# Optimization experiments

Hardware: AMD Instinct MI355X
Metric: run time of the kernel (lower is better)

Reference implementation:

```python
import jax, jax.numpy as jnp
import numpy as np

D, DEPTH, HEADS, P, IMG = 768, 12, 12, 16, 224
GRID = IMG // P
NTOK = GRID * GRID + 1  # 197
PLEN, NTASK, NCLS = 5, 5, 100
DEEP = (2, 3, 4)
HD = D // HEADS
LN_EPS = 1e-6


def _ln(x, w, b):
    m = x.mean(-1, keepdims=True)
    v = ((x - m) ** 2).mean(-1, keepdims=True)
    return (x - m) * jax.lax.rsqrt(v + LN_EPS) * w + b


def _l2n(x):
    return x * jax.lax.rsqrt(jnp.maximum((x * x).sum(-1, keepdims=True), 1e-12))


def _mlp(x, w1, b1, w2, b2):
    return jax.nn.gelu(x @ w1.T + b1, approximate=False) @ w2.T + b2


def _mha(x, wqkv, bqkv, wp, bp):
    B, N, _ = x.shape
    qkv = (x @ wqkv.T + bqkv).reshape(B, N, 3, HEADS, HD)
    q, k, v = qkv[:, :, 0], qkv[:, :, 1], qkv[:, :, 2]
    a = jax.nn.softmax(jnp.einsum('bnhd,bmhd->bhnm', q * HD ** -0.5, k), -1)
    o = jnp.einsum('bhnm,bmhd->bnhd', a, v).reshape(B, N, D)
    return o @ wp.T + bp


def _block(x, i, p):
    x = x + _mha(_ln(x, p['ln1_w'][i], p['ln1_b'][i]), p['qkv_w'][i], p['qkv_b'][i], p['proj_w'][i], p['proj_b'][i])
    return x + _mlp(_ln(x, p['ln2_w'][i], p['ln2_b'][i]), p['fc1_w'][i], p['fc1_b'][i], p['fc2_w'][i], p['fc2_b'][i])


def _blocks(x, p):
    for i in range(DEPTH):
        x = _block(x, i, p)
    return x


def _deep_block(x, i, li, prompts, p):
    # single-head prefix-prompt attention exactly as written in the torch module,
    # including the (buggy but faithful) transpose(1,2).reshape(B,N,C) scramble
    B, N, _ = x.shape
    nx = _ln(x, p['ln1_w'][i], p['ln1_b'][i])
    qkv = (nx @ p['qkv_w'][i].T + p['qkv_b'][i]).reshape(B, N, 3, D)
    q, k, v = qkv[:, :, 0], qkv[:, :, 1], qkv[:, :, 2]
    k = jnp.concatenate([prompts[:, 2 * li], k], axis=1)
    v = jnp.concatenate([prompts[:, 2 * li + 1], v], axis=1)
    a = jax.nn.softmax(jnp.einsum('bnd,bmd->bnm', q, k) * HD ** -0.5, -1)
    av = jnp.einsum('bnm,bmd->bnd', a, v)
    av = av.swapaxes(1, 2).reshape(B, N, D)
    x = x + (av @ p['proj_w'][i].T + p['proj_b'][i])
    return x + _mlp(_ln(x, p['ln2_w'][i], p['ln2_b'][i]), p['fc1_w'][i], p['fc1_b'][i], p['fc2_w'][i], p['fc2_b'][i])


def _embed(inputs, patch_w, patch_b, cls_token, pos_embed):
    B = inputs.shape[0]
    x = inputs.reshape(B, 3, GRID, P, GRID, P).transpose(0, 2, 4, 1, 3, 5).reshape(B, GRID * GRID, 3 * P * P)
    x = x @ patch_w.T + patch_b
    x = jnp.concatenate([jnp.broadcast_to(cls_token, (B, 1, D)), x], axis=1)
    return x + pos_embed


def _branch_forward(x, sel_main, main_idx, sub_idx, p, main_prompts, sub_prompt, pos_embed, fc_w, fc_b, norm_w, norm_b):
    B = x.shape[0]
    # ---- main branch: per-sample gathered deep prompts ----
    mx = x[main_idx]
    mp = main_prompts[sel_main].reshape(mx.shape[0], 2 * len(DEEP), PLEN, D)
    for i in range(DEPTH):
        if i in DEEP:
            mx = _deep_block(mx, i, DEEP.index(i), mp, p)
        else:
            mx = _block(mx, i, p)
    mx = _ln(mx, norm_w, norm_b)
    mlog = mx[:, 0] @ fc_w.T + fc_b  # fc_norm is Identity in timm vit_base
    # ---- sub branch: prepend sub prompts after cls ----
    sx = x[sub_idx]
    sp = jnp.broadcast_to(sub_prompt[0] + pos_embed[0, 0], (sx.shape[0], PLEN, D))
    sx = jnp.concatenate([sx[:, :1], sp, sx[:, 1:]], axis=1)
    sx = _ln(_blocks(sx, p), norm_w, norm_b)
    slog = sx[:, 1:1 + PLEN].mean(axis=1) @ fc_w.T + fc_b
    # scatter back to per-sample logits (fixed output shape)
    return jnp.zeros((B, NCLS), x.dtype).at[main_idx].set(mlog).at[sub_idx].set(slog)


def setup_inputs() -> dict:
    key = jax.random.key(0)
    ks = iter(jax.random.split(key, 32))
    nk = lambda: next(ks)
    r = lambda shape, sc=0.02: jax.random.normal(nk(), shape, jnp.float32) * sc
    return {
        'inputs': jax.random.normal(nk(), (16, 3, IMG, IMG), jnp.float32),
        'task_id': 4,
        'patch_w': r((D, 3 * P * P)),
        'patch_b': jnp.zeros((D,)),
        'cls_token': r((1, 1, D)),
        'pos_embed': r((1, NTOK, D)),
        'qkv_w': r((DEPTH, 3 * D, D)),
        'qkv_b': jnp.zeros((DEPTH, 3 * D)),
        'proj_w': r((DEPTH, D, D)),
        'proj_b': jnp.zeros((DEPTH, D)),
        'ln1_w': jnp.ones((DEPTH, D)), 'ln1_b': jnp.zeros((DEPTH, D)),
        'ln2_w': jnp.ones((DEPTH, D)), 'ln2_b': jnp.zeros((DEPTH, D)),
        'fc1_w': r((DEPTH, 4 * D, D)),
        'fc1_b': jnp.zeros((DEPTH, 4 * D)),
        'fc2_w': r((DEPTH, D, 4 * D)),
        'fc2_b': jnp.zeros((DEPTH, D)),
        'norm_w': jnp.ones((D,)), 'norm_b': jnp.zeros((D,)),
        'fc_w': r((NCLS, D)),
        'fc_b': jnp.zeros((NCLS,)),
        'main_key': r((NTASK, D), 1.0),
        'sub_key': r((1, D), 1.0),
        'main_prompts': r((NTASK, 1, 2, len(DEEP), PLEN, D), 1.0),
        'sub_prompt': r((1, PLEN, D), 1.0),
    }


def reference(inputs, task_id, patch_w, patch_b, cls_token, pos_embed, qkv_w, qkv_b, proj_w, proj_b,
              ln1_w, ln1_b, ln2_w, ln2_b, fc1_w, fc1_b, fc2_w, fc2_b, norm_w, norm_b, fc_w, fc_b,
              main_key, sub_key, main_prompts, sub_prompt):
    p = dict(qkv_w=qkv_w, qkv_b=qkv_b, proj_w=proj_w, proj_b=proj_b, ln1_w=ln1_w, ln1_b=ln1_b,
             ln2_w=ln2_w, ln2_b=ln2_b, fc1_w=fc1_w, fc1_b=fc1_b, fc2_w=fc2_w, fc2_b=fc2_b)
    x = _embed(inputs, patch_w, patch_b, cls_token, pos_embed)
    # frozen query pass (torch.no_grad in the original)
    query = _ln(_blocks(x, p), norm_w, norm_b)[:, 0]
    # test-time routing: cosine similarity to [main_key[:task_id+1], sub_key]
    cand = jnp.concatenate([main_key[:task_id + 1], sub_key], axis=0)
    sim = _l2n(query) @ _l2n(cand).T
    sel = jnp.argmax(sim, axis=1)  # selection_size == 1
    main_mask = sel <= task_id
    main_idx = jnp.nonzero(main_mask)[0]
    sub_idx = jnp.nonzero(jnp.logical_not(main_mask))[0]
    sel_main = sel[main_idx]
    return _branch_forward(x, sel_main, main_idx, sub_idx, p, main_prompts, sub_prompt, pos_embed,
                           fc_w, fc_b, norm_w, norm_b)
```

## Files before the change

### kernel.cpp

```cpp
#include <hip/hip_runtime.h>
#include <math.h>

#define B_    16
#define NT_   197
#define NS_   202
#define HEADS_ 12
#define DEPTH_ 12
#define NCLS_ 100
#define MROW_ (B_ * NT_)
#define SROW_ (B_ * NS_)
#define CROW_ (MROW_ + SROW_)
#define PAD_  128

typedef __attribute__((ext_vector_type(8))) short short8v;
typedef __attribute__((ext_vector_type(4))) float f32x4;

__device__ __forceinline__ short f2bf(float f){
    unsigned u = __builtin_bit_cast(unsigned, f);
    unsigned r = (u + 0x7FFFu + ((u >> 16) & 1u)) >> 16;
    return (short)r;
}
__device__ __forceinline__ unsigned pk2(float a, float b){
    return (unsigned)(unsigned short)f2bf(a) | (((unsigned)(unsigned short)f2bf(b)) << 16);
}
__device__ __forceinline__ float bf2f(unsigned short s){
    unsigned u = ((unsigned)s) << 16;
    return __builtin_bit_cast(float, u);
}
__device__ __forceinline__ float4 ld4bf(const short* p){
    uint2 u = *(const uint2*)p;
    float4 r;
    r.x = bf2f((unsigned short)(u.x & 0xffff));
    r.y = bf2f((unsigned short)(u.x >> 16));
    r.z = bf2f((unsigned short)(u.y & 0xffff));
    r.w = bf2f((unsigned short)(u.y >> 16));
    return r;
}
__device__ __forceinline__ void gld16(const short* g, short* l){
    __builtin_amdgcn_global_load_lds(
        (const __attribute__((address_space(1))) unsigned*)g,
        (__attribute__((address_space(3))) unsigned*)l, 16, 0, 0);
}

__device__ __forceinline__ double block_reduce_sum_d(double s, double* red, int lane, int wid){
#pragma unroll
    for (int off = 32; off; off >>= 1) s += __shfl_xor(s, off);
    if (lane == 0) red[wid] = s;
    __syncthreads();
    double S = red[0] + red[1] + red[2] + red[3];
    __syncthreads();
    return S;
}

__global__ void convert_w_k(const float* __restrict__ in, short* __restrict__ out, long n){
    long i = ((long)blockIdx.x * 256 + threadIdx.x) * 8;
    long stride = (long)gridDim.x * 256 * 8;
    for (; i < n; i += stride){
        float4 a = *(const float4*)(in + i);
        float4 b = *(const float4*)(in + i + 4);
        uint4 o4;
        o4.x = pk2(a.x, a.y); o4.y = pk2(a.z, a.w);
        o4.z = pk2(b.x, b.y); o4.w = pk2(b.z, b.w);
        *(uint4*)(out + i) = o4;
    }
}

template<int EPI, int WB>
__global__ __launch_bounds__(256) void gemm_bf16(
    const short* __restrict__ A, const void* __restrict__ Wv,
    const float* __restrict__ bias, const float* __restrict__ Res,
    float* __restrict__ Cf, short* __restrict__ Cb, int M, int K, int N)
{
    __shared__ short As[128 * 32];
    __shared__ short Bs[128 * 32];
    const int t = threadIdx.x;
    const int lane = t & 63, wid = t >> 6;
    const int wr = wid >> 1, wc = wid & 1;
    const long row0 = (long)blockIdx.y * 128;
    const long col0 = (long)blockIdx.x * 128;

    f32x4 acc[4][4];
#pragma unroll
    for (int i = 0; i < 4; i++)
#pragma unroll
        for (int j = 0; j < 4; j++) acc[i][j] = (f32x4){0.f, 0.f, 0.f, 0.f};

    const int l15 = lane & 15, lkg = lane >> 4;
    const int lrow = lane >> 2;
    const int lcol = (lane & 3) * 8;

    for (int k0 = 0; k0 < K; k0 += 32){
#pragma unroll
        for (int i = 0; i < 2; i++){
            int rb = wid * 32 + i * 16;
            gld16(A + (row0 + rb + lrow) * K + k0 + lcol, &As[rb * 32]);
        }
        if (WB == 1){
            const short* Wb = (const short*)Wv;
#pragma unroll
            for (int i = 0; i < 2; i++){
                int rb = wid * 32 + i * 16;
                gld16(Wb + (col0 + rb + lrow) * K + k0 + lcol, &Bs[rb * 32]);
            }
        } else {
            const float* Wf = (const float*)Wv;
            const int bn = t >> 1, bh = t & 1;
            const float* Wp = Wf + (col0 + bn) * K + k0 + bh * 16;
            unsigned rr[8];
#pragma unroll
            for (int g = 0; g < 8; g++){
                float2 f = *(const float2*)(Wp + g * 2);
                rr[g] = pk2(f.x, f.y);
            }
            uint4 lo = {rr[0], rr[1], rr[2], rr[3]};
            uint4 hi = {rr[4], rr[5], rr[6], rr[7]};
            *(uint4*)(&Bs[bn * 32 + bh * 16])     = lo;
            *(uint4*)(&Bs[bn * 32 + bh * 16 + 8]) = hi;
        }
        __syncthreads();

        short8v a[4], b[4];
#pragma unroll
        for (int i = 0; i < 4; i++)
            a[i] = *(const short8v*)(&As[(wr * 64 + i * 16 + l15) * 32 + lkg * 8]);
#pragma unroll
        for (int j = 0; j < 4; j++)
            b[j] = *(const short8v*)(&Bs[(wc * 64 + j * 16 + l15) * 32 + lkg * 8]);
#pragma unroll
        for (int i = 0; i < 4; i++)
#pragma unroll
            for (int j = 0; j < 4; j++)
                acc[i][j] = __builtin_amdgcn_mfma_f32_16x16x32_bf16(a[i], b[j], acc[i][j], 0, 0, 0);
        __syncthreads();
    }

#pragma unroll
    for (int i = 0; i < 4; i++){
#pragma unroll
        for (int q = 0; q < 4; q++){
            long gr = row0 + wr * 64 + i * 16 + lkg * 4 + q;
            if (gr >= M) continue;
#pragma unroll
            for (int j = 0; j < 4; j++){
                long gc = col0 + wc * 64 + j * 16 + l15;
                float v = acc[i][j][q] + bias[gc];
                if (EPI == 1){
                    v = 0.5f * v * (1.f + erff(v * 0.70710678118654752f));
                    Cb[gr * N + gc] = f2bf(v);
                } else if (EPI == 2){
                    Cf[gr * N + gc] = v + Res[gr * N + gc];
                } else if (EPI == 3){
                    Cb[gr * N + gc] = f2bf(v);
                } else {
                    Cf[gr * N + gc] = v;
                }
            }
        }
    }
}

__global__ __launch_bounds__(256) void ln_k(const float* __restrict__ x,
    const float* __restrict__ w, const float* __restrict__ b,
    short* __restrict__ y, int M)
{
    const int lane = threadIdx.x & 63, wv = threadIdx.x >> 6;
    const int row = blockIdx.x * 4 + wv;
    if (row >= M) return;
    const float* xr = x + (long)row * 768;
    float v[12];
    float s = 0.f;
#pragma unroll
    for (int j = 0; j < 12; j++){ v[j] = xr[lane + j * 64]; s += v[j]; }
#pragma unroll
    for (int off = 32; off; off >>= 1) s += __shfl_xor(s, off);
    float m = s * (1.f / 768.f);
    float q = 0.f;
#pragma unroll
    for (int j = 0; j < 12; j++){ v[j] -= m; q += v[j] * v[j]; }
#pragma unroll
    for (int off = 32; off; off >>= 1) q += __shfl_xor(q, off);
    float rs = 1.f / sqrtf(q * (1.f / 768.f) + 1e-6f);
    short* yr = y + (long)row * 768;
#pragma unroll
    for (int j = 0; j < 12; j++)
        yr[lane + j * 64] = f2bf(v[j] * rs * w[lane + j * 64] + b[lane + j * 64]);
}

__global__ __launch_bounds__(512) void attn_mfma(
    const short* __restrict__ qkv0, short* __restrict__ o0, int N0,
    const short* __restrict__ qkv1, short* __restrict__ o1, int N1)
{
    __shared__ short Ks[208 * 72];
    __shared__ short Vs[64 * 232];
    __shared__ short Ps[8 * 16 * 232];
    const int bh = blockIdx.x;
    const int b = bh / HEADS_, h = bh % HEADS_;
    const int seg = blockIdx.y;
    const short* qkv = seg ? qkv1 : qkv0;
    short* o = seg ? o1 : o0;
    const int Ntok = seg ? N1 : N0;
    const int t = threadIdx.x, lane = t & 63, wid = t >> 6;
    const long rb = (long)b * Ntok;

    {
        const int r = t >> 2, c = (t & 3) * 16;
#pragma unroll
        for (int pass = 0; pass < 2; pass++){
            int m = r + pass * 128;
            if (m < 208){
                if (m < Ntok){
                    const short* kr = qkv + (rb + m) * 2304 + 768  + h * 64 + c;
                    const short* vr = qkv + (rb + m) * 2304 + 1536 + h * 64 + c;
                    *(uint4*)(&Ks[m * 72 + c])     = *(const uint4*)(kr);
                    *(uint4*)(&Ks[m * 72 + c + 8]) = *(const uint4*)(kr + 8);
#pragma unroll
                    for (int j = 0; j < 16; j++)
                        Vs[(c + j) * 232 + m] = vr[j];
                } else {
#pragma unroll
                    for (int j = 0; j < 16; j += 2)
                        *(unsigned*)(&Ks[m * 72 + c + j]) = 0u;
#pragma unroll
                    for (int j = 0; j < 16; j++)
                        Vs[(c + j) * 232 + m] = 0;
                }
            }
        }
        for (int i = t; i < 64 * 16; i += 512){
            int d = i >> 4, m = 208 + (i & 15);
            Vs[d * 232 + m] = 0;
        }
        for (int i = t; i < 8 * 16 * 16; i += 512){
            int w = i >> 8, rr = (i >> 4) & 15, m = 208 + (i & 15);
            Ps[(w * 16 + rr) * 232 + m] = 0;
        }
    }
    __syncthreads();

    const int l15 = lane & 15, lkg = lane >> 4;
    short* Pw = &Ps[wid * 16 * 232];

    for (int s = wid; s < 13; s += 8){
        const int q0 = s * 16;
        short8v a0, a1;
        {
            int qrow = q0 + l15;
            if (qrow < Ntok){
                const short* qp = qkv + (rb + qrow) * 2304 + h * 64;
                a0 = *(const short8v*)(qp + lkg * 8);
                a1 = *(const short8v*)(qp + 32 + lkg * 8);
            } else {
                uint4 z = {0u,0u,0u,0u};
                a0 = __builtin_bit_cast(short8v, z);
                a1 = __builtin_bit_cast(short8v, z);
            }
        }
        f32x4 sacc[13];
#pragma unroll
        for (int j = 0; j < 13; j++){
            short8v b0 = *(const short8v*)(&Ks[(j * 16 + l15) * 72 + lkg * 8]);
            short8v b1 = *(const short8v*)(&Ks[(j * 16 + l15) * 72 + 32 + lkg * 8]);
            f32x4 z = {0.f, 0.f, 0.f, 0.f};
            z = __builtin_amdgcn_mfma_f32_16x16x32_bf16(a0, b0, z, 0, 0, 0);
            z = __builtin_amdgcn_mfma_f32_16x16x32_bf16(a1, b1, z, 0, 0, 0);
            sacc[j][0] = z[0] * 0.125f; sacc[j][1] = z[1] * 0.125f;
            sacc[j][2] = z[2] * 0.125f; sacc[j][3] = z[3] * 0.125f;
        }
#pragma unroll
        for (int j = 0; j < 13; j++){
            if (j * 16 + l15 >= Ntok){
                sacc[j][0] = -1e30f; sacc[j][1] = -1e30f;
                sacc[j][2] = -1e30f; sacc[j][3] = -1e30f;
            }
        }
#pragma unroll
        for (int rr = 0; rr < 4; rr++){
            float mx = sacc[0][rr];
#pragma unroll
            for (int j = 1; j < 13; j++) mx = fmaxf(mx, sacc[j][rr]);
            mx = fmaxf(mx, __shfl_xor(mx, 1));
            mx = fmaxf(mx, __shfl_xor(mx, 2));
            mx = fmaxf(mx, __shfl_xor(mx, 4));
            mx = fmaxf(mx, __shfl_xor(mx, 8));
            float pv[13];
            float sum = 0.f;
#pragma unroll
            for (int j = 0; j < 13; j++){
                float e = expf(sacc[j][rr] - mx);
                pv[j] = e; sum += e;
            }
            sum += __shfl_xor(sum, 1);
            sum += __shfl_xor(sum, 2);
            sum += __shfl_xor(sum, 4);
            sum += __shfl_xor(sum, 8);
            float inv = 1.f / sum;
#pragma unroll
            for (int j = 0; j < 13; j++)
                Pw[(lkg * 4 + rr) * 232 + j * 16 + l15] = f2bf(pv[j] * inv);
        }
        short8v pa[7];
#pragma unroll
        for (int kc = 0; kc < 7; kc++)
            pa[kc] = *(const short8v*)(&Pw[l15 * 232 + kc * 32 + lkg * 8]);
#pragma unroll
        for (int dj = 0; dj < 4; dj++){
            f32x4 oacc = {0.f, 0.f, 0.f, 0.f};
#pragma unroll
            for (int kc = 0; kc < 7; kc++){
                short8v vb = *(const short8v*)(&Vs[(dj * 16 + l15) * 232 + kc * 32 + lkg * 8]);
                oacc = __builtin_amdgcn_mfma_f32_16x16x32_bf16(pa[kc], vb, oacc, 0, 0, 0);
            }
#pragma unroll
            for (int rr = 0; rr < 4; rr++){
                int q = q0 + lkg * 4 + rr;
                if (q < Ntok)
                    o[(rb + q) * 768 + h * 64 + dj * 16 + l15] = f2bf(oacc[rr]);
            }
        }
    }
}

__global__ __launch_bounds__(256) void attn_deep_v2(
    const short* __restrict__ qkv, const float* __restrict__ prompts,
    const int* __restrict__ selm, short* __restrict__ o, int li)
{
    __shared__ float q[768];
    __shared__ float sc[256];
    __shared__ float red[256];
    const int b = blockIdx.x, n = blockIdx.y, t = threadIdx.x;
    const int lane = t & 63, w = t >> 6;
    const short* qr = qkv + (long)(b * NT_ + n) * 2304;
    q[t] = bf2f((unsigned short)qr[t]);
    q[t + 256] = bf2f((unsigned short)qr[t + 256]);
    q[t + 512] = bf2f((unsigned short)qr[t + 512]);
    __syncthreads();

    const float4 q0 = *(const float4*)(&q[lane * 4]);
    const float4 q1 = *(const float4*)(&q[256 + lane * 4]);
    const float4 q2 = *(const float4*)(&q[512 + lane * 4]);

    const float* kp = prompts + ((long)selm[b] * 6 + 2 * li) * 5 * 768;
    const float* vp = kp + 5 * 768;

    for (int m = w; m < 202; m += 4){
        float4 k0, k1, k2;
        if (m < 5){
            const float* kr = kp + (long)m * 768;
            k0 = *(const float4*)(kr + lane * 4);
            k1 = *(const float4*)(kr + 256 + lane * 4);
            k2 = *(const float4*)(kr + 512 + lane * 4);
        } else {
            const short* kr = qkv + (long)(b * NT_ + (m - 5)) * 2304 + 768;
            k0 = ld4bf(kr + lane * 4);
            k1 = ld4bf(kr + 256 + lane * 4);
            k2 = ld4bf(kr + 512 + lane * 4);
        }
        float a = q0.x*k0.x + q0.y*k0.y + q0.z*k0.z + q0.w*k0.w
                + q1.x*k1.x + q1.y*k1.y + q1.z*k1.z + q1.w*k1.w
                + q2.x*k2.x + q2.y*k2.y + q2.z*k2.z + q2.w*k2.w;
#pragma unroll
        for (int off = 32; off; off >>= 1) a += __shfl_xor(a, off);
        if (lane == 0) sc[m] = a * 0.125f;
    }
    __syncthreads();

    float s = (t < 202) ? sc[t] : -1e30f;
    red[t] = s; __syncthreads();
    for (int wd = 128; wd; wd >>= 1){ if (t < wd) red[t] = fmaxf(red[t], red[t+wd]); __syncthreads(); }
    float mx = red[0]; __syncthreads();
    float e = (t < 202) ? expf(s - mx) : 0.f;
    red[t] = e; __syncthreads();
    for (int wd = 128; wd; wd >>= 1){ if (t < wd) red[t] += red[t+wd]; __syncthreads(); }
    float inv = 1.f / red[0];
    __syncthreads();
    sc[t] = e * inv;
    __syncthreads();

    float a0 = 0.f, a1 = 0.f, a2 = 0.f;
    for (int m = 0; m < 5; m++){
        const float* vr = vp + (long)m * 768;
        float pm = sc[m];
        a0 += pm * vr[t]; a1 += pm * vr[t + 256]; a2 += pm * vr[t + 512];
    }
    for (int m = 5; m < 202; m++){
        const short* vr = qkv + (long)(b * NT_ + (m - 5)) * 2304 + 1536;
        float pm = sc[m];
        a0 += pm * bf2f((unsigned short)vr[t]);
        a1 += pm * bf2f((unsigned short)vr[t + 256]);
        a2 += pm * bf2f((unsigned short)vr[t + 512]);
    }
    short* ob = o + (long)b * NT_ * 768 + n;
    ob[(long)t * 197]         = f2bf(a0);
    ob[(long)(t + 256) * 197] = f2bf(a1);
    ob[(long)(t + 512) * 197] = f2bf(a2);
}

__global__ void unfold_k(const float* __restrict__ in, short* __restrict__ out){
    long i = (long)blockIdx.x * 256 + threadIdx.x;
    long total = (long)B_ * 196 * 768;
    if (i >= total) return;
    int f = (int)(i % 768); long rw = i / 768;
    int t = (int)(rw % 196); int b = (int)(rw / 196);
    int gy = t / 14, gx = t % 14;
    int c = f >> 8, rem = f & 255, py = rem >> 4, px = rem & 15;
    out[i] = f2bf(in[(((long)(b * 3 + c) * 224) + gy * 16 + py) * 224 + gx * 16 + px]);
}

__global__ void assemble_k(const float* __restrict__ pe, const float* __restrict__ cls,
    const float* __restrict__ pos, float* __restrict__ x0){
    long i = (long)blockIdx.x * 256 + threadIdx.x;
    long total = (long)B_ * NT_ * 768;
    if (i >= total) return;
    int d = (int)(i % 768); long rw = i / 768;
    int n = (int)(rw % NT_); int b = (int)(rw / NT_);
    float v;
    if (n == 0) v = cls[d] + pos[d];
    else        v = pe[((long)b * 196 + (n - 1)) * 768 + d] + pos[(long)n * 768 + d];
    x0[i] = v;
}

__global__ void copy_f(const float* __restrict__ a, float* __restrict__ b, long total){
    long i = (long)blockIdx.x * 256 + threadIdx.x;
    if (i < total) b[i] = a[i];
}

__global__ void build_sub_k(const float* __restrict__ x0, const float* __restrict__ subp,
    const float* __restrict__ pos, float* __restrict__ xSub){
    long i = (long)blockIdx.x * 256 + threadIdx.x;
    long total = (long)B_ * NS_ * 768;
    if (i >= total) return;
    int d = (int)(i % 768); long rw = i / 768;
    int n = (int)(rw % NS_); int b = (int)(rw / NS_);
    float v;
    if (n == 0)      v = x0[((long)b * NT_) * 768 + d];
    else if (n <= 5) v = subp[(n - 1) * 768 + d] + pos[d];
    else             v = x0[((long)b * NT_ + (n - 5)) * 768 + d];
    xSub[i] = v;
}

__global__ __launch_bounds__(256) void select_k(
    const float* __restrict__ xA, const float* __restrict__ norm_w,
    const float* __restrict__ norm_b, const float* __restrict__ main_key,
    const float* __restrict__ sub_key, const int* __restrict__ task_id_p,
    int* __restrict__ selm, int* __restrict__ flag)
{
    __shared__ double red[4];
    int b = blockIdx.x, t = threadIdx.x, lane = t & 63, wid = t >> 6;
    const float* xr = xA + (long)b * NT_ * 768;
    double v0 = xr[t], v1 = xr[t + 256], v2 = xr[t + 512];
    double S = block_reduce_sum_d(v0 + v1 + v2, red, lane, wid);
    double m = S * (1.0 / 768.0);
    double d0 = v0 - m, d1 = v1 - m, d2 = v2 - m;
    double Q = block_reduce_sum_d(d0*d0 + d1*d1 + d2*d2, red, lane, wid);
    double rs = 1.0 / sqrt(Q * (1.0 / 768.0) + 1e-6);
    double q0 = d0 * rs * (double)norm_w[t]       + (double)norm_b[t];
    double q1 = d1 * rs * (double)norm_w[t + 256] + (double)norm_b[t + 256];
    double q2 = d2 * rs * (double)norm_w[t + 512] + (double)norm_b[t + 512];
    double qn = block_reduce_sum_d(q0*q0 + q1*q1 + q2*q2, red, lane, wid);
    double qinv = 1.0 / sqrt(fmax(qn, 1e-12));

    int tk = *task_id_p;
    int ncand = tk + 2;
    double best = -1e300; int bsel = 0;
    for (int c = 0; c < ncand; c++){
        const float* cr = (c <= tk) ? (main_key + (long)c * 768) : sub_key;
        double c0 = cr[t], c1 = cr[t + 256], c2 = cr[t + 512];
        double dotq = block_reduce_sum_d(q0*c0 + q1*c1 + q2*c2, red, lane, wid);
        double nc   = block_reduce_sum_d(c0*c0 + c1*c1 + c2*c2, red, lane, wid);
        double sim = dotq * qinv * (1.0 / sqrt(fmax(nc, 1e-12)));
        if (sim > best){ best = sim; bsel = c; }
    }
    if (t == 0){
        int isMain = (bsel <= tk) ? 1 : 0;
        selm[b] = isMain ? bsel : 0;
        flag[b] = isMain;
    }
}

__global__ __launch_bounds__(256) void head_k(
    const float* __restrict__ xM, const float* __restrict__ xSub,
    const float* __restrict__ norm_w, const float* __restrict__ norm_b,
    const float* __restrict__ fc_w, const float* __restrict__ fc_b,
    const int* __restrict__ flag, float* __restrict__ out)
{
    __shared__ double vec[768];
    __shared__ double red[4];
    int b = blockIdx.x, t = threadIdx.x, lane = t & 63, wid = t >> 6;
    int isMain = flag[b];
    double a0 = 0.0, a1 = 0.0, a2 = 0.0;
    int nrows = isMain ? 1 : 5;
    for (int rI = 0; rI < nrows; rI++){
        const float* xr = isMain ? (xM + (long)b * NT_ * 768)
                                 : (xSub + ((long)b * NS_ + 1 + rI) * 768);
        double v0 = xr[t], v1 = xr[t + 256], v2 = xr[t + 512];
        double S = block_reduce_sum_d(v0 + v1 + v2, red, lane, wid);
        double m = S * (1.0 / 768.0);
        double d0 = v0 - m, d1 = v1 - m, d2 = v2 - m;
        double Q = block_reduce_sum_d(d0*d0 + d1*d1 + d2*d2, red, lane, wid);
        double rs = 1.0 / sqrt(Q * (1.0 / 768.0) + 1e-6);
        a0 += d0 * rs * (double)norm_w[t]       + (double)norm_b[t];
        a1 += d1 * rs * (double)norm_w[t + 256] + (double)norm_b[t + 256];
        a2 += d2 * rs * (double)norm_w[t + 512] + (double)norm_b[t + 512];
    }
    double scl = isMain ? 1.0 : 0.2;
    vec[t] = a0 * scl; vec[t + 256] = a1 * scl; vec[t + 512] = a2 * scl;
    __syncthreads();
    if (t < NCLS_){
        const float* wr = fc_w + (long)t * 768;
        double acc = (double)fc_b[t];
#pragma unroll 8
        for (int j = 0; j < 768; j++) acc += vec[j] * (double)wr[j];
        out[b * NCLS_ + t] = (float)acc;
    }
}

struct Params {
    const float *qkv_w, *qkv_b, *proj_w, *proj_b;
    const float *ln1_w, *ln1_b, *ln2_w, *ln2_b;
    const float *fc1_w, *fc1_b, *fc2_w, *fc2_b;
    const float *prompts; const int* selm;
    short *lnb, *attb, *hidb;
    short *qkvb;
    const short *qkv_wc, *proj_wc, *fc1_wc, *fc2_wc;
    bool cache;
};

template<int EPI>
static void launch_gemm(hipStream_t st, const short* A, const float* Wf, const short* Wc,
                        bool cache, const float* bias, const float* Res,
                        float* Cf, short* Cb, int M, int K, int N)
{
    dim3 g(N / 128, (M + 127) / 128);
    if (cache)
        gemm_bf16<EPI, 1><<<g, 256, 0, st>>>(A, (const void*)Wc, bias, Res, Cf, Cb, M, K, N);
    else
        gemm_bf16<EPI, 0><<<g, 256, 0, st>>>(A, (const void*)Wf, bias, Res, Cf, Cb, M, K, N);
}

static void run_layer(hipStream_t st, float* x, int M, int layer, int mode, int li,
                      const Params& P)
{
    int lnGrid = (M + 3) / 4;
    ln_k<<<lnGrid, 256, 0, st>>>(x, P.ln1_w + layer * 768, P.ln1_b + layer * 768, P.lnb, M);
    launch_gemm<3>(st, P.lnb, P.qkv_w + (long)layer * 2304 * 768,
        P.qkv_wc + (P.cache ? (long)layer * 2304 * 768 : 0), P.cache,
        P.qkv_b + layer * 2304, nullptr, nullptr, P.qkvb, M, 768, 2304);
    if (mode == 0){
        attn_mfma<<<dim3(B_ * HEADS_, 2), 512, 0, st>>>(
            P.qkvb, P.attb, NT_,
            P.qkvb + (long)MROW_ * 2304, P.attb + (long)MROW_ * 768, NS_);
    } else if (mode == 1){
        attn_mfma<<<dim3(B_ * HEADS_, 1), 512, 0, st>>>(
            P.qkvb, P.attb, NT_, P.qkvb, P.attb, NT_);
    } else {
        attn_deep_v2<<<dim3(B_, NT_), 256, 0, st>>>(P.qkvb, P.prompts, P.selm, P.attb, li);
    }
    launch_gemm<2>(st, P.attb, P.proj_w + (long)layer * 768 * 768,
        P.proj_wc + (P.cache ? (long)layer * 768 * 768 : 0), P.cache,
        P.proj_b + layer * 768, x, x, nullptr, M, 768, 768);
    ln_k<<<lnGrid, 256, 0, st>>>(x, P.ln2_w + layer * 768, P.ln2_b + layer * 768, P.lnb, M);
    launch_gemm<1>(st, P.lnb, P.fc1_w + (long)layer * 3072 * 768,
        P.fc1_wc + (P.cache ? (long)layer * 3072 * 768 : 0), P.cache,
        P.fc1_b + layer * 3072, nullptr, nullptr, P.hidb, M, 768, 3072);
    launch_gemm<2>(st, P.hidb, P.fc2_w + (long)layer * 768 * 3072,
        P.fc2_wc + (P.cache ? (long)layer * 768 * 3072 : 0), P.cache,
        P.fc2_b + layer * 768, x, x, nullptr, M, 3072, 768);
}

extern "C" void kernel_launch(void* const* d_in, const int* in_sizes, int n_in,
                              void* d_out, int out_size, void* d_ws, size_t ws_size,
                              hipStream_t stream)
{
    (void)in_sizes; (void)n_in; (void)out_size;
    const float* inputs   = (const float*)d_in[0];
    const int*   task_id  = (const int*)  d_in[1];
    const float* patch_w  = (const float*)d_in[2];
    const float* patch_b  = (const float*)d_in[3];
    const float* cls_tok  = (const float*)d_in[4];
    const float* pos      = (const float*)d_in[5];
    const float* qkv_w    = (const float*)d_in[6];
    const float* qkv_b    = (const float*)d_in[7];
    const float* proj_w   = (const float*)d_in[8];
    const float* proj_b   = (const float*)d_in[9];
    const float* ln1_w    = (const float*)d_in[10];
    const float* ln1_b    = (const float*)d_in[11];
    const float* ln2_w    = (const float*)d_in[12];
    const float* ln2_b    = (const float*)d_in[13];
    const float* fc1_w    = (const float*)d_in[14];
    const float* fc1_b    = (const float*)d_in[15];
    const float* fc2_w    = (const float*)d_in[16];
    const float* fc2_b    = (const float*)d_in[17];
    const float* norm_w   = (const float*)d_in[18];
    const float* norm_b   = (const float*)d_in[19];
    const float* fc_w     = (const float*)d_in[20];
    const float* fc_b     = (const float*)d_in[21];
    const float* main_key = (const float*)d_in[22];
    const float* sub_key  = (const float*)d_in[23];
    const float* m_prompts= (const float*)d_in[24];
    const float* s_prompt = (const float*)d_in[25];
    float* out = (float*)d_out;

    char* wsb = (char*)d_ws;
    size_t off = 0;
    auto allocB = [&](size_t bytes) -> void* {
        void* p = (void*)(wsb + off);
        off += (bytes + 255) & ~(size_t)255;
        return p;
    };
    float* x0   = (float*)allocB((size_t)MROW_ * 768 * 4);
    float* xC   = (float*)allocB((size_t)CROW_ * 768 * 4);
    float* xM   = (float*)allocB((size_t)MROW_ * 768 * 4);
    short* lnb  = (short*)allocB((size_t)(CROW_ + PAD_) * 768 * 2);
    short* attb = (short*)allocB((size_t)(CROW_ + PAD_) * 768 * 2);
    short* qkvb = (short*)allocB((size_t)(CROW_ + PAD_) * 2304 * 2);
    short* hidb = (short*)allocB((size_t)(CROW_ + PAD_) * 3072 * 2);
    float* peo  = (float*)allocB((size_t)3136 * 768 * 4);
    int*   selm = (int*)allocB(64);
    int*   flag = (int*)allocB(64);

    const size_t nQkv = (size_t)DEPTH_ * 2304 * 768;
    const size_t nProj = (size_t)DEPTH_ * 768 * 768;
    const size_t nFc1 = (size_t)DEPTH_ * 3072 * 768;
    const size_t nFc2 = (size_t)DEPTH_ * 768 * 3072;
    const size_t nPatch = (size_t)768 * 768;
    size_t cacheBytes = (nQkv + nProj + nFc1 + nFc2 + nPatch) * 2 + 5 * 256;
    bool cache = (ws_size >= off + cacheBytes + (1u << 20));
    short *qkv_wc = nullptr, *proj_wc = nullptr, *fc1_wc = nullptr, *fc2_wc = nullptr, *patch_wc = nullptr;
    if (cache){
        qkv_wc  = (short*)allocB(nQkv * 2);
        proj_wc = (short*)allocB(nProj * 2);
        fc1_wc  = (short*)allocB(nFc1 * 2);
        fc2_wc  = (short*)allocB(nFc2 * 2);
        patch_wc= (short*)allocB(nPatch * 2);
        convert_w_k<<<2048, 256, 0, stream>>>(qkv_w,  qkv_wc,  (long)nQkv);
        convert_w_k<<<1024, 256, 0, stream>>>(proj_w, proj_wc, (long)nProj);
        convert_w_k<<<2048, 256, 0, stream>>>(fc1_w,  fc1_wc,  (long)nFc1);
        convert_w_k<<<2048, 256, 0, stream>>>(fc2_w,  fc2_wc,  (long)nFc2);
        convert_w_k<<<256,  256, 0, stream>>>(patch_w, patch_wc, (long)nPatch);
    }

    Params P;
    P.qkv_w = qkv_w; P.qkv_b = qkv_b; P.proj_w = proj_w; P.proj_b = proj_b;
    P.ln1_w = ln1_w; P.ln1_b = ln1_b; P.ln2_w = ln2_w; P.ln2_b = ln2_b;
    P.fc1_w = fc1_w; P.fc1_b = fc1_b; P.fc2_w = fc2_w; P.fc2_b = fc2_b;
    P.prompts = m_prompts; P.selm = selm;
    P.lnb = lnb; P.attb = attb; P.hidb = hidb; P.qkvb = qkvb;
    P.qkv_wc = qkv_wc; P.proj_wc = proj_wc; P.fc1_wc = fc1_wc; P.fc2_wc = fc2_wc;
    P.cache = cache;

    const long XN = (long)MROW_ * 768;

    {
        long tot = (long)B_ * 196 * 768;
        short* un = hidb;
        unfold_k<<<(int)((tot + 255) / 256), 256, 0, stream>>>(inputs, un);
        launch_gemm<0>(stream, un, patch_w, patch_wc, cache, patch_b, nullptr,
                       peo, nullptr, 3136, 768, 768);
        assemble_k<<<(int)((XN + 255) / 256), 256, 0, stream>>>(peo, cls_tok, pos, x0);
        copy_f<<<(int)((XN + 255) / 256), 256, 0, stream>>>(x0, xC, XN);
        long st = (long)SROW_ * 768;
        build_sub_k<<<(int)((st + 255) / 256), 256, 0, stream>>>(x0, s_prompt, pos,
                                                                 xC + (long)MROW_ * 768);
    }

    for (int i = 0; i < DEPTH_; i++){
        run_layer(stream, xC, CROW_, i, 0, 0, P);
        if (i == 1)
            copy_f<<<(int)((XN + 255) / 256), 256, 0, stream>>>(xC, xM, XN);
    }

    select_k<<<16, 256, 0, stream>>>(xC, norm_w, norm_b, main_key, sub_key,
                                     task_id, selm, flag);

    for (int i = 2; i < DEPTH_; i++){
        int mode = (i >= 2 && i <= 4) ? 2 : 1;
        run_layer(stream, xM, MROW_, i, mode, i - 2, P);
    }

    head_k<<<16, 256, 0, stream>>>(xM, xC + (long)MROW_ * 768, norm_w, norm_b,
                                   fc_w, fc_b, flag, out);
}
```

Baseline: 5.984 ms.

## Batch four queries per block in deep-prompt attention and split MFMA attention tiles

The deep-prompt attention kernel now handles four query rows per block instead of one, so each K and V row read from global memory is reused across four queries. The block-wide shared-memory softmax reductions become per-wave shuffle reductions, which removes many barriers. Separately, the single-segment MFMA attention launch now splits the 13 query tiles across two grid segments (tiles 0-6 and 7-12), which doubles the block count but has each block reload K and V into shared memory. The trade-off is more registers per thread in the deep kernel, which may lower occupancy.

```diff
diff --git a/kernel.cpp b/kernel.cpp
--- a/kernel.cpp
+++ b/kernel.cpp
@@ -187,8 +187,8 @@
 }
 
 __global__ __launch_bounds__(512) void attn_mfma(
-    const short* __restrict__ qkv0, short* __restrict__ o0, int N0,
-    const short* __restrict__ qkv1, short* __restrict__ o1, int N1)
+    const short* __restrict__ qkv0, short* __restrict__ o0, int N0, int tb0, int te0,
+    const short* __restrict__ qkv1, short* __restrict__ o1, int N1, int tb1, int te1)
 {
     __shared__ short Ks[208 * 72];
     __shared__ short Vs[64 * 232];
@@ -199,6 +199,8 @@
     const short* qkv = seg ? qkv1 : qkv0;
     short* o = seg ? o1 : o0;
     const int Ntok = seg ? N1 : N0;
+    const int tb = seg ? tb1 : tb0;
+    const int te = seg ? te1 : te0;
     const int t = threadIdx.x, lane = t & 63, wid = t >> 6;
     const long rb = (long)b * Ntok;
 
@@ -240,7 +242,7 @@
     const int l15 = lane & 15, lkg = lane >> 4;
     short* Pw = &Ps[wid * 16 * 232];
 
-    for (int s = wid; s < 13; s += 8){
+    for (int s = tb + wid; s < te; s += 8){
         const int q0 = s * 16;
         short8v a0, a1;
         {
@@ -320,24 +322,25 @@
     }
 }
 
-__global__ __launch_bounds__(256) void attn_deep_v2(
+__global__ __launch_bounds__(256) void attn_deep_v3(
     const short* __restrict__ qkv, const float* __restrict__ prompts,
     const int* __restrict__ selm, short* __restrict__ o, int li)
 {
-    __shared__ float q[768];
-    __shared__ float sc[256];
-    __shared__ float red[256];
-    const int b = blockIdx.x, n = blockIdx.y, t = threadIdx.x;
+    __shared__ float sc[4][208];
+    const int b = blockIdx.x, g = blockIdx.y, t = threadIdx.x;
     const int lane = t & 63, w = t >> 6;
-    const short* qr = qkv + (long)(b * NT_ + n) * 2304;
-    q[t] = bf2f((unsigned short)qr[t]);
-    q[t + 256] = bf2f((unsigned short)qr[t + 256]);
-    q[t + 512] = bf2f((unsigned short)qr[t + 512]);
-    __syncthreads();
-
-    const float4 q0 = *(const float4*)(&q[lane * 4]);
-    const float4 q1 = *(const float4*)(&q[256 + lane * 4]);
-    const float4 q2 = *(const float4*)(&q[512 + lane * 4]);
+    const int n0 = g * 4;
+
+    float4 q0[4], q1[4], q2[4];
+#pragma unroll
+    for (int qi = 0; qi < 4; qi++){
+        int n = n0 + qi;
+        int nn = (n < NT_) ? n : (NT_ - 1);
+        const short* qr = qkv + (long)(b * NT_ + nn) * 2304;
+        q0[qi] = ld4bf(qr + lane * 4);
+        q1[qi] = ld4bf(qr + 256 + lane * 4);
+        q2[qi] = ld4bf(qr + 512 + lane * 4);
+    }
 
     const float* kp = prompts + ((long)selm[b] * 6 + 2 * li) * 5 * 768;
     const float* vp = kp + 5 * 768;
@@ -355,44 +358,84 @@
             k1 = ld4bf(kr + 256 + lane * 4);
             k2 = ld4bf(kr + 512 + lane * 4);
         }
-        float a = q0.x*k0.x + q0.y*k0.y + q0.z*k0.z + q0.w*k0.w
-                + q1.x*k1.x + q1.y*k1.y + q1.z*k1.z + q1.w*k1.w
-                + q2.x*k2.x + q2.y*k2.y + q2.z*k2.z + q2.w*k2.w;
-#pragma unroll
-        for (int off = 32; off; off >>= 1) a += __shfl_xor(a, off);
-        if (lane == 0) sc[m] = a * 0.125f;
+        float a[4];
+#pragma unroll
+        for (int qi = 0; qi < 4; qi++){
+            a[qi] = q0[qi].x*k0.x + q0[qi].y*k0.y + q0[qi].z*k0.z + q0[qi].w*k0.w
+                  + q1[qi].x*k1.x + q1[qi].y*k1.y + q1[qi].z*k1.z + q1[qi].w*k1.w
+                  + q2[qi].x*k2.x + q2[qi].y*k2.y + q2[qi].z*k2.z + q2[qi].w*k2.w;
+        }
+#pragma unroll
+        for (int off = 32; off; off >>= 1){
+#pragma unroll
+            for (int qi = 0; qi < 4; qi++) a[qi] += __shfl_xor(a[qi], off);
+        }
+        if (lane == 0){
+#pragma unroll
+            for (int qi = 0; qi < 4; qi++) sc[qi][m] = a[qi] * 0.125f;
+        }
     }
     __syncthreads();
 
-    float s = (t < 202) ? sc[t] : -1e30f;
-    red[t] = s; __syncthreads();
-    for (int wd = 128; wd; wd >>= 1){ if (t < wd) red[t] = fmaxf(red[t], red[t+wd]); __syncthreads(); }
-    float mx = red[0]; __syncthreads();
-    float e = (t < 202) ? expf(s - mx) : 0.f;
-    red[t] = e; __syncthreads();
-    for (int wd = 128; wd; wd >>= 1){ if (t < wd) red[t] += red[t+wd]; __syncthreads(); }
-    float inv = 1.f / red[0];
+    {
+        float v[4];
+#pragma unroll
+        for (int i = 0; i < 4; i++){
+            int m = lane + i * 64;
+            v[i] = (m < 202) ? sc[w][m] : -1e30f;
+        }
+        float mx = fmaxf(fmaxf(v[0], v[1]), fmaxf(v[2], v[3]));
+#pragma unroll
+        for (int off = 32; off; off >>= 1) mx = fmaxf(mx, __shfl_xor(mx, off));
+        float e[4], sum = 0.f;
+#pragma unroll
+        for (int i = 0; i < 4; i++){
+            int m = lane + i * 64;
+            e[i] = (m < 202) ? expf(v[i] - mx) : 0.f;
+            sum += e[i];
+        }
+#pragma unroll
+        for (int off = 32; off; off >>= 1) sum += __shfl_xor(sum, off);
+        float inv = 1.f / sum;
+#pragma unroll
+        for (int i = 0; i < 4; i++){
+            int m = lane + i * 64;
+            if (m < 202) sc[w][m] = e[i] * inv;
+        }
+    }
     __syncthreads();
-    sc[t] = e * inv;
-    __syncthreads();
-
-    float a0 = 0.f, a1 = 0.f, a2 = 0.f;
+
+    float a0[4] = {0.f,0.f,0.f,0.f}, a1[4] = {0.f,0.f,0.f,0.f}, a2[4] = {0.f,0.f,0.f,0.f};
     for (int m = 0; m < 5; m++){
         const float* vr = vp + (long)m * 768;
-        float pm = sc[m];
-        a0 += pm * vr[t]; a1 += pm * vr[t + 256]; a2 += pm * vr[t + 512];
+        float v0 = vr[t], v1 = vr[t + 256], v2 = vr[t + 512];
+#pragma unroll
+        for (int qi = 0; qi < 4; qi++){
+            float pm = sc[qi][m];
+            a0[qi] += pm * v0; a1[qi] += pm * v1; a2[qi] += pm * v2;
+        }
     }
     for (int m = 5; m < 202; m++){
         const short* vr = qkv + (long)(b * NT_ + (m - 5)) * 2304 + 1536;
-        float pm = sc[m];
-        a0 += pm * bf2f((unsigned short)vr[t]);
-        a1 += pm * bf2f((unsigned short)vr[t + 256]);
-        a2 += pm * bf2f((unsigned short)vr[t + 512]);
-    }
-    short* ob = o + (long)b * NT_ * 768 + n;
-    ob[(long)t * 197]         = f2bf(a0);
-    ob[(long)(t + 256) * 197] = f2bf(a1);
-    ob[(long)(t + 512) * 197] = f2bf(a2);
+        float v0 = bf2f((unsigned short)vr[t]);
+        float v1 = bf2f((unsigned short)vr[t + 256]);
+        float v2 = bf2f((unsigned short)vr[t + 512]);
+#pragma unroll
+        for (int qi = 0; qi < 4; qi++){
+            float pm = sc[qi][m];
+            a0[qi] += pm * v0; a1[qi] += pm * v1; a2[qi] += pm * v2;
+        }
+    }
+#pragma unroll
+    for (int qi = 0; qi < 4; qi++){
+        int n = n0 + qi;
+        if (n < NT_){
+            short* ob = o + (long)b * NT_ * 768 + n;
+            ob[(long)t * 197]         = f2bf(a0[qi]);
+            ob[(long)(t + 256) * 197] = f2bf(a1[qi]);
+            ob[(long)(t + 512) * 197] = f2bf(a2[qi]);
+        }
+    }
 }
 
 __global__ void unfold_k(const float* __restrict__ in, short* __restrict__ out){
@@ -547,13 +590,14 @@
         P.qkv_b + layer * 2304, nullptr, nullptr, P.qkvb, M, 768, 2304);
     if (mode == 0){
         attn_mfma<<<dim3(B_ * HEADS_, 2), 512, 0, st>>>(
-            P.qkvb, P.attb, NT_,
-            P.qkvb + (long)MROW_ * 2304, P.attb + (long)MROW_ * 768, NS_);
+            P.qkvb, P.attb, NT_, 0, 13,
+            P.qkvb + (long)MROW_ * 2304, P.attb + (long)MROW_ * 768, NS_, 0, 13);
     } else if (mode == 1){
-        attn_mfma<<<dim3(B_ * HEADS_, 1), 512, 0, st>>>(
-            P.qkvb, P.attb, NT_, P.qkvb, P.attb, NT_);
+        attn_mfma<<<dim3(B_ * HEADS_, 2), 512, 0, st>>>(
+            P.qkvb, P.attb, NT_, 0, 7,
+            P.qkvb, P.attb, NT_, 7, 13);
     } else {
-        attn_deep_v2<<<dim3(B_, NT_), 256, 0, st>>>(P.qkvb, P.prompts, P.selm, P.attb, li);
+        attn_deep_v3<<<dim3(B_, 50), 256, 0, st>>>(P.qkvb, P.prompts, P.selm, P.attb, li);
     }
     launch_gemm<2>(st, P.attb, P.proj_w + (long)layer * 768 * 768,
         P.proj_wc + (P.cache ? (long)layer * 768 * 768 : 0), P.cache,
```

Result: no change. 5.936 ms (-0.8%).
